# Optimization experiments

Hardware: AMD Instinct MI355X
Metric: run time of the kernel (lower is better)

Reference implementation:

```python
import jax, jax.numpy as jnp
import numpy as np

B, T, D = 2, 2048, 1024
NH, NKV, HD, RD = 16, 4, 64, 32


def apply_rope(x, cos, sin):
    # x: [B, H, T, hd]; cos/sin: [T, 1, 1, RD//2]
    r = cos.shape[-1] * 2
    x1 = x[..., : r // 2]
    x2 = x[..., r // 2 : r]
    x_pass = x[..., r:]
    c = cos.reshape(1, 1, cos.shape[0], -1)  # [1,1,T,RD//2]
    s = sin.reshape(1, 1, sin.shape[0], -1)
    return jnp.concatenate([x1 * c - x2 * s, x1 * s + x2 * c, x_pass], axis=-1)


def setup_inputs() -> dict:
    key = jax.random.key(0)
    ks = jax.random.split(key, 8)
    # realistic partial-RoPE angle tables
    inv_freq = 1.0 / (10000.0 ** (np.arange(0, RD, 2, dtype=np.float32) / RD))
    ang = np.arange(T, dtype=np.float32)[:, None] * inv_freq[None, :]  # [T, RD//2]
    cos = jnp.asarray(np.cos(ang)).reshape(T, 1, 1, RD // 2)
    sin = jnp.asarray(np.sin(ang)).reshape(T, 1, 1, RD // 2)
    return {
        "x": jax.random.normal(ks[0], (B, T, D), dtype=jnp.float32),
        "cos": cos,
        "sin": sin,
        "v0": jax.random.normal(ks[1], (B, NH, T, HD), dtype=jnp.float32),
        "Wqkv": jax.random.normal(ks[2], ((NH + 2 * NKV) * HD, D), dtype=jnp.float32) * (D ** -0.5),
        "Wproj": jax.random.normal(ks[3], (D, D), dtype=jnp.float32) * (D ** -0.5),
        "vrl_alpha": jnp.full((NH,), 0.1, dtype=jnp.float32),
        "qk_scale": 0.5 + jax.random.uniform(ks[4], (NH,), dtype=jnp.float32),
    }


def reference(x, cos, sin, v0, Wqkv, Wproj, vrl_alpha, qk_scale):
    nH, nKV, hd = NH, NKV, HD
    qkv = jnp.einsum("btd,ed->bte", x, Wqkv)  # [B,T,(nH+2nKV)*hd]
    q = qkv[..., : nH * hd].reshape(B, T, nH, hd).transpose(0, 2, 1, 3)
    k = qkv[..., nH * hd : (nH + nKV) * hd].reshape(B, T, nKV, hd).transpose(0, 2, 1, 3)
    v = qkv[..., (nH + nKV) * hd :].reshape(B, T, nKV, hd).transpose(0, 2, 1, 3)
    q = apply_rope(q, cos, sin)
    k = apply_rope(k, cos, sin)
    reps = nH // nKV
    k_exp = jnp.repeat(k, reps, axis=1)  # [B,nH,T,hd]
    v_exp = jnp.repeat(v, reps, axis=1)
    # VRL blend (layer_idx > 0)
    alpha = jax.nn.sigmoid(vrl_alpha)[None, :, None, None]
    v_exp = (1.0 - alpha) * v_exp + alpha * v0
    # per-head learned qk scale, split as sqrt on q and k
    sfac = jnp.sqrt(qk_scale[None, :, None, None] * (hd ** -0.5))
    q_s = q * sfac
    k_s = k_exp * sfac
    # causal SDPA (default scale 1/sqrt(hd))
    scores = jnp.einsum("bhqd,bhkd->bhqk", q_s, k_s) * (hd ** -0.5)
    causal = jnp.tril(jnp.ones((T, T), dtype=bool))
    scores = jnp.where(causal[None, None], scores, jnp.float32(-1e30))
    attn = jax.nn.softmax(scores, axis=-1)
    y = jnp.einsum("bhqk,bhkd->bhqd", attn, v_exp)
    y = y.transpose(0, 2, 1, 3).reshape(B, T, D)
    out = jnp.einsum("btd,ed->bte", y, Wproj)
    return out, v0
```

## Files before the change

kernel.cpp:

```cpp
#include <hip/hip_runtime.h>
#include <hip/hip_bf16.h>

#define B_   2
#define T_   2048
#define D_   1024
#define NH_  16
#define NKV_ 4
#define HD_  64
#define E_   1536
#define LOG2E 1.4426950408889634f

typedef __attribute__((ext_vector_type(8))) __bf16 bf16x8;
typedef __attribute__((ext_vector_type(4))) __bf16 bf16x4;
typedef __attribute__((ext_vector_type(4))) float f32x4;

static __device__ __forceinline__ void gld_lds16(const unsigned short* g, unsigned short* l) {
  __builtin_amdgcn_global_load_lds(
      (const __attribute__((address_space(1))) unsigned int*)(unsigned long long)(const void*)g,
      (__attribute__((address_space(3))) unsigned int*)(unsigned int)(unsigned long long)(void*)l,
      16, 0, 0);
}

static __device__ __forceinline__ float fexp2(float x) {
  float r; asm("v_exp_f32 %0, %1" : "=v"(r) : "v"(x)); return r;
}
static __device__ __forceinline__ float fmax3(float a, float b, float c) {
  float r; asm("v_max3_f32 %0, %1, %2, %3" : "=v"(r) : "v"(a), "v"(b), "v"(c)); return r;
}
static __device__ __forceinline__ float frcp(float x) {
  float r; asm("v_rcp_f32 %0, %1" : "=v"(r) : "v"(x)); return r;
}

#define CVT8(dst, f0, f1) {                                                    \
  dst[0] = (__bf16)f0.x; dst[1] = (__bf16)f0.y;                               \
  dst[2] = (__bf16)f0.z; dst[3] = (__bf16)f0.w;                               \
  dst[4] = (__bf16)f1.x; dst[5] = (__bf16)f1.y;                               \
  dst[6] = (__bf16)f1.z; dst[7] = (__bf16)f1.w; }

__global__ void k_convert_all(const float* __restrict__ x, const float* __restrict__ wq,
                              const float* __restrict__ wp,
                              unsigned short* __restrict__ xb, unsigned short* __restrict__ wqb,
                              unsigned short* __restrict__ wpb) {
  int i = blockIdx.x * blockDim.x + threadIdx.x;
  const float* src; unsigned short* dst; int j;
  if (i < 524288)      { src = x;  dst = xb;  j = i; }
  else if (i < 720896) { src = wq; dst = wqb; j = i - 524288; }
  else                 { src = wp; dst = wpb; j = i - 720896; }
  int n = j >> 7, c8 = (j & 127) * 8;
  const float4* p = (const float4*)(src + (size_t)n * 1024 + c8);
  float4 a = p[0], b = p[1];
  bf16x8 o; CVT8(o, a, b);
  *(bf16x8*)(dst + (size_t)n * 1024 + (c8 ^ ((n & 7) * 8))) = o;
}

__global__ __launch_bounds__(256) void k_gemm_qkv(
    const unsigned short* __restrict__ A,
    const unsigned short* __restrict__ W,
    const float* __restrict__ cosT, const float* __restrict__ sinT,
    const float* __restrict__ v0,
    const float* __restrict__ vrl, const float* __restrict__ qks,
    unsigned short* __restrict__ qb, unsigned short* __restrict__ kb,
    unsigned short* __restrict__ vb) {
  __shared__ __align__(16) unsigned short As[2][128 * 64];
  __shared__ __align__(16) unsigned short Ws[2][64 * 64];
  int tid = threadIdx.x;
  int w = tid >> 6, l = tid & 63, lo = l & 15, hi = l >> 4;
  int f = blockIdx.y * 24 + blockIdx.x;
  int f2 = (f & 7) * 96 + (f >> 3);
  int bn = f2 % 24, bm = f2 / 24;
  int rsw = (lo & 7) * 8;

  const unsigned short* Ab = A + (size_t)bm * 128 * 1024;
  const unsigned short* Wb = W + (size_t)bn * 64 * 1024;

  f32x4 acc[2][4];
#pragma unroll
  for (int mi = 0; mi < 2; ++mi)
#pragma unroll
    for (int ni = 0; ni < 4; ++ni) acc[mi][ni] = (f32x4){0.f, 0.f, 0.f, 0.f};

#define STAGE(kt, buf) {                                                       \
  int k0 = (kt) * 64;                                                         \
  _Pragma("unroll") for (int ii = 0; ii < 4; ++ii) {                          \
    int sb = ii * 256 + w * 64;                                               \
    gld_lds16(Ab + (size_t)((sb + l) >> 3) * 1024 + k0 + ((sb + l) & 7) * 8,  \
              &As[buf][sb * 8]); }                                            \
  _Pragma("unroll") for (int ii = 0; ii < 2; ++ii) {                          \
    int sb = ii * 256 + w * 64;                                               \
    gld_lds16(Wb + (size_t)((sb + l) >> 3) * 1024 + k0 + ((sb + l) & 7) * 8,  \
              &Ws[buf][sb * 8]); } }

  STAGE(0, 0);
  __syncthreads();

  for (int kt = 0; kt < 16; ++kt) {
    int cur = kt & 1;
    bool pf = (kt + 1) < 16;
    if (pf) STAGE(kt + 1, cur ^ 1);
    __builtin_amdgcn_s_setprio(1);
#pragma unroll
    for (int kk = 0; kk < 2; ++kk) {
      int c0 = (kk * 32 + hi * 8) ^ rsw;
      bf16x8 af0 = *(const bf16x8*)&As[cur][(w * 32 + lo) * 64 + c0];
      bf16x8 af1 = *(const bf16x8*)&As[cur][(w * 32 + 16 + lo) * 64 + c0];
#pragma unroll
      for (int ni = 0; ni < 4; ++ni) {
        bf16x8 wf = *(const bf16x8*)&Ws[cur][(ni * 16 + lo) * 64 + c0];
        acc[0][ni] = __builtin_amdgcn_mfma_f32_16x16x32_bf16(af0, wf, acc[0][ni], 0, 0, 0);
        acc[1][ni] = __builtin_amdgcn_mfma_f32_16x16x32_bf16(af1, wf, acc[1][ni], 0, 0, 0);
      }
    }
    __builtin_amdgcn_s_setprio(0);
    __syncthreads();
  }
#undef STAGE

  if (bn < 20) {
    int isq = (bn < 16);
    int h = isq ? bn : bn - 16;
    float sc = isq ? (qks[h] * (LOG2E / 64.0f)) : 1.0f;
    unsigned short* base = isq ? qb : kb;
    int nheads = isq ? NH_ : NKV_;
#pragma unroll
    for (int mi = 0; mi < 2; ++mi) {
#pragma unroll
      for (int r = 0; r < 4; ++r) {
        int row = bm * 128 + w * 32 + mi * 16 + hi * 4 + r;
        int b = row >> 11, t = row & 2047;
        float c = cosT[t * 16 + lo], s = sinT[t * 16 + lo];
        float a0 = acc[mi][0][r], a1 = acc[mi][1][r];
        __bf16* dp = (__bf16*)(base + ((size_t)(b * nheads + h) * T_ + t) * 64);
        int ts = isq ? 0 : (8 * (t & 7));
        dp[lo ^ ts]        = (__bf16)((a0 * c - a1 * s) * sc);
        dp[(16 + lo) ^ ts] = (__bf16)((a0 * s + a1 * c) * sc);
        dp[(32 + lo) ^ ts] = (__bf16)(acc[mi][2][r] * sc);
        dp[(48 + lo) ^ ts] = (__bf16)(acc[mi][3][r] * sc);
      }
    }
  } else {
    int hv = bn - 20;
    float av[4];
#pragma unroll
    for (int j = 0; j < 4; ++j) av[j] = 1.0f / (1.0f + __expf(-vrl[hv * 4 + j]));
#pragma unroll
    for (int mi = 0; mi < 2; ++mi) {
      int t0g = bm * 128 + w * 32 + mi * 16 + hi * 4;
      int b = t0g >> 11, t0 = t0g & 2047;
#pragma unroll
      for (int ni = 0; ni < 4; ++ni) {
        int d = ni * 16 + lo;
#pragma unroll
        for (int j = 0; j < 4; ++j) {
          float a = av[j], na = 1.0f - a;
          const float* v0p = v0 + ((size_t)(b * NH_ + hv * 4 + j) * T_ + t0) * 64 + d;
          bf16x4 vv;
#pragma unroll
          for (int r = 0; r < 4; ++r)
            vv[r] = (__bf16)(na * acc[mi][ni][r] + a * v0p[(size_t)r * 64]);
          *(bf16x4*)((unsigned short*)vb + ((size_t)(b * NH_ + hv * 4 + j) * 64 + d) * T_ +
                     (t0 ^ (8 * (lo & 7)))) = vv;
        }
      }
    }
  }
}

__global__ __launch_bounds__(256) void k_gemm_proj(
    const unsigned short* __restrict__ A,
    const unsigned short* __restrict__ W,
    const float* __restrict__ v0,
    float* __restrict__ C, float* __restrict__ out2) {
  __shared__ __align__(16) unsigned short As[2][128 * 64];
  __shared__ __align__(16) unsigned short Ws[2][64 * 64];
  int tid = threadIdx.x;

  if (blockIdx.y >= 32) {
    int idx = ((blockIdx.y - 32) * 16 + blockIdx.x) * 256 + tid;
    const float4* src = (const float4*)v0;
    float4* dst = (float4*)out2;
#pragma unroll
    for (int i = 0; i < 32; ++i) dst[idx + i * 32768] = src[idx + i * 32768];
    return;
  }

  int w = tid >> 6, l = tid & 63, lo = l & 15, hi = l >> 4;
  int f = blockIdx.y * 16 + blockIdx.x;
  int f2 = (f & 7) * 64 + (f >> 3);
  int bn = f2 & 15, bm = f2 >> 4;
  int rsw = (lo & 7) * 8;

  const unsigned short* Ab = A + (size_t)bm * 128 * 1024;
  const unsigned short* Wb = W + (size_t)bn * 64 * 1024;

  f32x4 acc[2][4];
#pragma unroll
  for (int mi = 0; mi < 2; ++mi)
#pragma unroll
    for (int ni = 0; ni < 4; ++ni) acc[mi][ni] = (f32x4){0.f, 0.f, 0.f, 0.f};

#define STAGE(kt, buf) {                                                       \
  int k0 = (kt) * 64;                                                         \
  _Pragma("unroll") for (int ii = 0; ii < 4; ++ii) {                          \
    int sb = ii * 256 + w * 64;                                               \
    gld_lds16(Ab + (size_t)((sb + l) >> 3) * 1024 + k0 + ((sb + l) & 7) * 8,  \
              &As[buf][sb * 8]); }                                            \
  _Pragma("unroll") for (int ii = 0; ii < 2; ++ii) {                          \
    int sb = ii * 256 + w * 64;                                               \
    gld_lds16(Wb + (size_t)((sb + l) >> 3) * 1024 + k0 + ((sb + l) & 7) * 8,  \
              &Ws[buf][sb * 8]); } }

  STAGE(0, 0);
  __syncthreads();
  for (int kt = 0; kt < 16; ++kt) {
    int cur = kt & 1;
    bool pf = (kt + 1) < 16;
    if (pf) STAGE(kt + 1, cur ^ 1);
    __builtin_amdgcn_s_setprio(1);
#pragma unroll
    for (int kk = 0; kk < 2; ++kk) {
      int c0 = (kk * 32 + hi * 8) ^ rsw;
      bf16x8 af0 = *(const bf16x8*)&As[cur][(w * 32 + lo) * 64 + c0];
      bf16x8 af1 = *(const bf16x8*)&As[cur][(w * 32 + 16 + lo) * 64 + c0];
#pragma unroll
      for (int ni = 0; ni < 4; ++ni) {
        bf16x8 wf = *(const bf16x8*)&Ws[cur][(ni * 16 + lo) * 64 + c0];
        acc[0][ni] = __builtin_amdgcn_mfma_f32_16x16x32_bf16(af0, wf, acc[0][ni], 0, 0, 0);
        acc[1][ni] = __builtin_amdgcn_mfma_f32_16x16x32_bf16(af1, wf, acc[1][ni], 0, 0, 0);
      }
    }
    __builtin_amdgcn_s_setprio(0);
    __syncthreads();
  }
#undef STAGE

#pragma unroll
  for (int mi = 0; mi < 2; ++mi) {
#pragma unroll
    for (int r = 0; r < 4; ++r) {
      int row = bm * 128 + w * 32 + mi * 16 + hi * 4 + r;
      float* cp = C + (size_t)row * D_ + bn * 64 + lo;
#pragma unroll
      for (int ni = 0; ni < 4; ++ni) cp[ni * 16] = acc[mi][ni][r];
    }
  }
}

static __device__ __forceinline__ void stage_kv8(const unsigned short* Kb, const unsigned short* Vb,
                                                 int kv0, int w, int l,
                                                 unsigned short* KsB, unsigned short* VsB) {
  gld_lds16(Kb + (size_t)kv0 * 64 + w * 512 + l * 8, KsB + w * 512);
  gld_lds16(Vb + (size_t)(w * 8 + (l >> 3)) * T_ + kv0 + (l & 7) * 8, VsB + w * 512);
}

__device__ __forceinline__ void softmax_state(f32x4 (&s)[4], float& m, float& lsum,
                                              f32x4 (&y)[4], unsigned short* PsW,
                                              int lo, int hi, int swz) {
  float a0 = fmax3(s[0][0], s[0][1], s[0][2]);
  float a1 = fmax3(s[0][3], s[1][0], s[1][1]);
  float a2 = fmax3(s[1][2], s[1][3], s[2][0]);
  float a3 = fmax3(s[2][1], s[2][2], s[2][3]);
  float a4 = fmax3(s[3][0], s[3][1], s[3][2]);
  float pm = fmaxf(fmax3(a0, a1, a2), fmax3(a3, a4, s[3][3]));
  if (!__all(pm <= m + 8.0f)) {
    pm = fmaxf(pm, __shfl_xor(pm, 16));
    pm = fmaxf(pm, __shfl_xor(pm, 32));
    float mnew = fmaxf(m, pm);
    float sc = fexp2(m - mnew);
    lsum *= sc;
#pragma unroll
    for (int r = 0; r < 4; ++r) {
      float scr = __shfl(sc, hi * 4 + r);
#pragma unroll
      for (int nf = 0; nf < 4; ++nf) y[nf][r] *= scr;
    }
    m = mnew;
  }
  float rs = 0.f;
#pragma unroll
  for (int nt = 0; nt < 4; ++nt) {
    float p0 = fexp2(s[nt][0] - m);
    float p1 = fexp2(s[nt][1] - m);
    float p2 = fexp2(s[nt][2] - m);
    float p3 = fexp2(s[nt][3] - m);
    rs += (p0 + p1) + (p2 + p3);
    bf16x4 pk;
    pk[0] = (__bf16)p0; pk[1] = (__bf16)p1; pk[2] = (__bf16)p2; pk[3] = (__bf16)p3;
    *(bf16x4*)(PsW + lo * 64 + ((nt * 16 + hi * 4) ^ swz)) = pk;
  }
  lsum += rs;
}

__global__ __launch_bounds__(512, 4) void k_attn(const unsigned short* __restrict__ Q,
                                                 const unsigned short* __restrict__ Kp,
                                                 const unsigned short* __restrict__ Vtp,
                                                 unsigned short* __restrict__ Y) {
  int p = blockIdx.x, h = blockIdx.y, b = blockIdx.z;
  if (b == 1) p = 15 - p;
  int tid = threadIdx.x;
  int w = tid >> 6, l = tid & 63, lo = l & 15, hi = l >> 4;
  int kh = h >> 2;
  int qtA = p, qtB = 31 - p;
  int ntB = qtB + 1;
  int st = w >> 2, wq = w & 3;
  int qt = st ? qtA : qtB;
  int q0 = qt * 64 + wq * 16;
  int swz = 8 * (lo & 7);

  __shared__ __align__(16) unsigned short Ks[2][4096];
  __shared__ __align__(16) unsigned short Vs[2][4096];
  __shared__ __align__(16) unsigned short Ps[8192];
  unsigned short* PsW = &Ps[w * 1024];

  const unsigned short* Qb = Q + ((size_t)(b * NH_ + h) * T_) * 64;
  const unsigned short* Kb = Kp + ((size_t)(b * NKV_ + kh) * T_) * 64;
  const unsigned short* Vb = Vtp + ((size_t)(b * NH_ + h) * 64) * T_;

  bf16x8 q_0 = *(const bf16x8*)(Qb + (size_t)(q0 + lo) * 64 + hi * 8);
  bf16x8 q_1 = *(const bf16x8*)(Qb + (size_t)(q0 + lo) * 64 + 32 + hi * 8);

  f32x4 y[4];
#pragma unroll
  for (int nf = 0; nf < 4; ++nf) y[nf] = (f32x4){0.f, 0.f, 0.f, 0.f};
  float m = -INFINITY, lsum = 0.f;

  stage_kv8(Kb, Vb, 0, w, l, Ks[0], Vs[0]);
  __syncthreads();
  int cur = 0;

  for (int kt = 0; kt < ntB; ++kt) {
    bool pf = (kt + 1) < ntB;
    if (pf) stage_kv8(Kb, Vb, (kt + 1) * 64, w, l, Ks[cur ^ 1], Vs[cur ^ 1]);

    if (kt <= qt) {
      int kv0 = kt * 64;
      const unsigned short* KsC = Ks[cur];
      const unsigned short* VsC = Vs[cur];

      f32x4 s[4];
      __builtin_amdgcn_s_setprio(1);
#pragma unroll
      for (int nt = 0; nt < 4; ++nt) {
        int rrow = (nt * 16 + lo) * 64;
        int c0 = (hi * 8) ^ swz;
        bf16x8 kf0 = *(const bf16x8*)&KsC[rrow + c0];
        bf16x8 kf1 = *(const bf16x8*)&KsC[rrow + (c0 ^ 32)];
        f32x4 a = (f32x4){0.f, 0.f, 0.f, 0.f};
        a = __builtin_amdgcn_mfma_f32_16x16x32_bf16(kf0, q_0, a, 0, 0, 0);
        a = __builtin_amdgcn_mfma_f32_16x16x32_bf16(kf1, q_1, a, 0, 0, 0);
        s[nt] = a;
      }
      __builtin_amdgcn_s_setprio(0);

      if (kt == qt) {
#pragma unroll
        for (int nt = 0; nt < 4; ++nt)
#pragma unroll
          for (int r = 0; r < 4; ++r)
            if (kv0 + nt * 16 + hi * 4 + r > q0 + lo) s[nt][r] = -1e30f;
      }

      softmax_state(s, m, lsum, y, PsW, lo, hi, swz);

      __builtin_amdgcn_s_setprio(1);
#pragma unroll
      for (int kc = 0; kc < 2; ++kc) {
        int pcol = (kc * 32 + hi * 8) ^ swz;
        bf16x8 pa = *(const bf16x8*)&PsW[lo * 64 + pcol];
#pragma unroll
        for (int nf = 0; nf < 4; ++nf) {
          bf16x8 vf = *(const bf16x8*)&VsC[(nf * 16 + lo) * 64 + pcol];
          y[nf] = __builtin_amdgcn_mfma_f32_16x16x32_bf16(pa, vf, y[nf], 0, 0, 0);
        }
      }
      __builtin_amdgcn_s_setprio(0);
    }

    __syncthreads();
    cur ^= 1;
  }

  lsum += __shfl_xor(lsum, 16);
  lsum += __shfl_xor(lsum, 32);
  float inv = frcp(lsum);
#pragma unroll
  for (int r = 0; r < 4; ++r) {
    float iv = __shfl(inv, hi * 4 + r);
    int t = q0 + hi * 4 + r;
    int sw = 8 * (t & 7);
    __bf16* yp = (__bf16*)(Y + ((size_t)(b * T_ + t)) * D_ + h * 64);
#pragma unroll
    for (int nf = 0; nf < 4; ++nf)
      yp[(nf * 16 + lo) ^ sw] = (__bf16)(y[nf][r] * iv);
  }
}

extern "C" void kernel_launch(void* const* d_in, const int* in_sizes, int n_in,
                              void* d_out, int out_size, void* d_ws, size_t ws_size,
                              hipStream_t stream) {
  const float* x     = (const float*)d_in[0];
  const float* cosT  = (const float*)d_in[1];
  const float* sinT  = (const float*)d_in[2];
  const float* v0    = (const float*)d_in[3];
  const float* Wqkv  = (const float*)d_in[4];
  const float* Wproj = (const float*)d_in[5];
  const float* vrl   = (const float*)d_in[6];
  const float* qks   = (const float*)d_in[7];
  float* out = (float*)d_out;

  char* ws = (char*)d_ws;
  unsigned short* xb     = (unsigned short*)ws;
  unsigned short* wqkvb  = (unsigned short*)(ws + 8388608);
  unsigned short* wprojb = (unsigned short*)(ws + 11534336);
  unsigned short* qb     = (unsigned short*)(ws + 13631488);
  unsigned short* kb     = (unsigned short*)(ws + 22020096);
  unsigned short* vb     = (unsigned short*)(ws + 24117248);
  unsigned short* yb     = (unsigned short*)(ws + 32505856);

  k_convert_all<<<3328, 256, 0, stream>>>(x, Wqkv, Wproj, xb, wqkvb, wprojb);

  k_gemm_qkv<<<dim3(24, 32), 256, 0, stream>>>(xb, wqkvb, cosT, sinT, v0, vrl, qks, qb, kb, vb);

  k_attn<<<dim3(16, NH_, B_), 512, 0, stream>>>(qb, kb, vb, yb);

  k_gemm_proj<<<dim3(16, 40), 256, 0, stream>>>(yb, wprojb, v0, out, out + 4194304);
}
```

Measured before the change: 96.20 us.

## Triple-buffer LDS staging with partial vmcnt waits in GEMMs and attention

Replaces double-buffered global-to-LDS staging with a three-stage ring in both GEMM kernels and the attention kernel. Each iteration waits only for the oldest outstanding loads via an explicit vmcnt count plus a single barrier, so two tiles stay in flight while compute runs. The attention kernel's launch-bounds occupancy hint drops from 4 to 2 blocks per CU to allow the larger LDS footprint. This raises LDS usage and may cut occupancy, and correctness relies on the hard-coded vmcnt values matching the number of loads each stage issues.

Result: slower. 99.21 us (+3.1%).

```diff
diff --git a/kernel.cpp b/kernel.cpp
--- a/kernel.cpp
+++ b/kernel.cpp
@@ -30,6 +30,11 @@
 static __device__ __forceinline__ float frcp(float x) {
   float r; asm("v_rcp_f32 %0, %1" : "=v"(r) : "v"(x)); return r;
 }
+
+#define PIPE_BARRIER(N) {                                   \
+  asm volatile("s_waitcnt vmcnt(" #N ")" ::: "memory");     \
+  __builtin_amdgcn_s_barrier();                             \
+  __builtin_amdgcn_sched_barrier(0); }
 
 #define CVT8(dst, f0, f1) {                                                    \
   dst[0] = (__bf16)f0.x; dst[1] = (__bf16)f0.y;                               \
@@ -61,8 +66,8 @@
     const float* __restrict__ vrl, const float* __restrict__ qks,
     unsigned short* __restrict__ qb, unsigned short* __restrict__ kb,
     unsigned short* __restrict__ vb) {
-  __shared__ __align__(16) unsigned short As[2][128 * 64];
-  __shared__ __align__(16) unsigned short Ws[2][64 * 64];
+  __shared__ __align__(16) unsigned short As[3][128 * 64];
+  __shared__ __align__(16) unsigned short Ws[3][64 * 64];
   int tid = threadIdx.x;
   int w = tid >> 6, l = tid & 63, lo = l & 15, hi = l >> 4;
   int f = blockIdx.y * 24 + blockIdx.x;
@@ -90,13 +95,12 @@
     gld_lds16(Wb + (size_t)((sb + l) >> 3) * 1024 + k0 + ((sb + l) & 7) * 8,  \
               &Ws[buf][sb * 8]); } }
 
-  STAGE(0, 0);
-  __syncthreads();
+  STAGE(0, 0); STAGE(1, 1);
+  int cur = 0, wb = 2;
 
   for (int kt = 0; kt < 16; ++kt) {
-    int cur = kt & 1;
-    bool pf = (kt + 1) < 16;
-    if (pf) STAGE(kt + 1, cur ^ 1);
+    if (kt + 1 < 16) PIPE_BARRIER(6) else PIPE_BARRIER(0);
+    if (kt + 2 < 16) STAGE(kt + 2, wb);
     __builtin_amdgcn_s_setprio(1);
 #pragma unroll
     for (int kk = 0; kk < 2; ++kk) {
@@ -111,7 +115,8 @@
       }
     }
     __builtin_amdgcn_s_setprio(0);
-    __syncthreads();
+    cur = (cur == 2) ? 0 : cur + 1;
+    wb = (wb == 2) ? 0 : wb + 1;
   }
 #undef STAGE
 
@@ -170,8 +175,8 @@
     const unsigned short* __restrict__ W,
     const float* __restrict__ v0,
     float* __restrict__ C, float* __restrict__ out2) {
-  __shared__ __align__(16) unsigned short As[2][128 * 64];
-  __shared__ __align__(16) unsigned short Ws[2][64 * 64];
+  __shared__ __align__(16) unsigned short As[3][128 * 64];
+  __shared__ __align__(16) unsigned short Ws[3][64 * 64];
   int tid = threadIdx.x;
 
   if (blockIdx.y >= 32) {
@@ -209,12 +214,12 @@
     gld_lds16(Wb + (size_t)((sb + l) >> 3) * 1024 + k0 + ((sb + l) & 7) * 8,  \
               &Ws[buf][sb * 8]); } }
 
-  STAGE(0, 0);
-  __syncthreads();
+  STAGE(0, 0); STAGE(1, 1);
+  int cur = 0, wb = 2;
+
   for (int kt = 0; kt < 16; ++kt) {
-    int cur = kt & 1;
-    bool pf = (kt + 1) < 16;
-    if (pf) STAGE(kt + 1, cur ^ 1);
+    if (kt + 1 < 16) PIPE_BARRIER(6) else PIPE_BARRIER(0);
+    if (kt + 2 < 16) STAGE(kt + 2, wb);
     __builtin_amdgcn_s_setprio(1);
 #pragma unroll
     for (int kk = 0; kk < 2; ++kk) {
@@ -229,7 +234,8 @@
       }
     }
     __builtin_amdgcn_s_setprio(0);
-    __syncthreads();
+    cur = (cur == 2) ? 0 : cur + 1;
+    wb = (wb == 2) ? 0 : wb + 1;
   }
 #undef STAGE
 
@@ -290,7 +296,7 @@
   lsum += rs;
 }
 
-__global__ __launch_bounds__(512, 4) void k_attn(const unsigned short* __restrict__ Q,
+__global__ __launch_bounds__(512, 2) void k_attn(const unsigned short* __restrict__ Q,
                                                  const unsigned short* __restrict__ Kp,
                                                  const unsigned short* __restrict__ Vtp,
                                                  unsigned short* __restrict__ Y) {
@@ -306,8 +312,8 @@
   int q0 = qt * 64 + wq * 16;
   int swz = 8 * (lo & 7);
 
-  __shared__ __align__(16) unsigned short Ks[2][4096];
-  __shared__ __align__(16) unsigned short Vs[2][4096];
+  __shared__ __align__(16) unsigned short Ks[3][4096];
+  __shared__ __align__(16) unsigned short Vs[3][4096];
   __shared__ __align__(16) unsigned short Ps[8192];
   unsigned short* PsW = &Ps[w * 1024];
 
@@ -324,12 +330,12 @@
   float m = -INFINITY, lsum = 0.f;
 
   stage_kv8(Kb, Vb, 0, w, l, Ks[0], Vs[0]);
-  __syncthreads();
-  int cur = 0;
+  stage_kv8(Kb, Vb, 64, w, l, Ks[1], Vs[1]);
+  int cur = 0, wbuf = 2;
 
   for (int kt = 0; kt < ntB; ++kt) {
-    bool pf = (kt + 1) < ntB;
-    if (pf) stage_kv8(Kb, Vb, (kt + 1) * 64, w, l, Ks[cur ^ 1], Vs[cur ^ 1]);
+    if (kt + 1 < ntB) PIPE_BARRIER(2) else PIPE_BARRIER(0);
+    if (kt + 2 < ntB) stage_kv8(Kb, Vb, (kt + 2) * 64, w, l, Ks[wbuf], Vs[wbuf]);
 
     if (kt <= qt) {
       int kv0 = kt * 64;
@@ -375,8 +381,8 @@
       __builtin_amdgcn_s_setprio(0);
     }
 
-    __syncthreads();
-    cur ^= 1;
+    cur = (cur == 2) ? 0 : cur + 1;
+    wbuf = (wbuf == 2) ? 0 : wbuf + 1;
   }
 
   lsum += __shfl_xor(lsum, 16);
```
